# Kernel tuning notes

Hardware: AMD Instinct MI355X
Metric: run time of the kernel (lower is better)

The kernel has to match this reference:

```python
import jax, jax.numpy as jnp
import numpy as np

N_QUBITS = 4
LAYERS = 1

# state has shape [N] + [2]*n; qubit w lives on axis w+1 (wire 0 = most significant, as in PennyLane)

def _apply_ry(state, theta, w, n):
    s0 = jnp.take(state, 0, axis=w + 1)
    s1 = jnp.take(state, 1, axis=w + 1)
    shp = (-1,) + (1,) * (n - 1)
    c = jnp.cos(theta / 2).reshape(shp)
    s = jnp.sin(theta / 2).reshape(shp)
    return jnp.stack([c * s0 - s * s1, s * s0 + c * s1], axis=w + 1)


def _apply_crx(state, theta, ctrl, tgt, n):
    sub0 = jnp.take(state, 0, axis=ctrl + 1)  # control = 0 subspace (unchanged)
    sub1 = jnp.take(state, 1, axis=ctrl + 1)  # control = 1 subspace -> RX on target
    t_ax = tgt + 1 if tgt < ctrl else tgt     # target axis inside sub1 ([N] at axis 0)
    a0 = jnp.take(sub1, 0, axis=t_ax)
    a1 = jnp.take(sub1, 1, axis=t_ax)
    shp = (-1,) + (1,) * (n - 2)
    c = jnp.cos(theta / 2).reshape(shp).astype(state.dtype)
    s = jnp.sin(theta / 2).reshape(shp).astype(state.dtype)
    new1 = jnp.stack([c * a0 - 1j * s * a1, -1j * s * a0 + c * a1], axis=t_ax)
    return jnp.stack([sub0, new1], axis=ctrl + 1)


def run_circuit(params):
    """Ansatz 14 (arXiv:1905.10876) applied to |0...0>, batched over tokens. params: [N, 4*n*layers]."""
    n = N_QUBITS
    N = params.shape[0]
    state = jnp.zeros((N,) + (2,) * n, jnp.complex64)
    state = state.at[(slice(None),) + (0,) * n].set(1.0)
    idx = 0
    for _ in range(LAYERS):
        for i in range(n):
            state = _apply_ry(state, params[:, idx], i, n); idx += 1
        for i in range(n - 1, -1, -1):
            state = _apply_crx(state, params[:, idx], i, (i + 1) % n, n); idx += 1
        for i in range(n):
            state = _apply_ry(state, params[:, idx], i, n); idx += 1
        for i in [n - 1] + list(range(n - 1)):
            state = _apply_crx(state, params[:, idx], i, (i - 1) % n, n); idx += 1
    return state


def measure_xyz(state, n):
    """<X_w>, <Y_w>, <Z_w> for all wires; order matches the PennyLane qnode (all X, all Y, all Z)."""
    N = state.shape[0]
    xs, ys, zs = [], [], []
    for w in range(n):
        s0 = jnp.take(state, 0, axis=w + 1).reshape(N, -1)
        s1 = jnp.take(state, 1, axis=w + 1).reshape(N, -1)
        prod = jnp.sum(jnp.conj(s0) * s1, axis=-1)
        xs.append(2.0 * jnp.real(prod))
        ys.append(2.0 * jnp.imag(prod))
        zs.append(jnp.sum(jnp.abs(s0) ** 2 - jnp.abs(s1) ** 2, axis=-1))
    return jnp.stack(xs + ys + zs, axis=-1)  # [N, 3n]


def setup_inputs() -> dict:
    key = jax.random.key(0)
    k = jax.random.split(key, 7)
    B, L, S, H, E = 2, 2048, 2048, 8, 64
    n_params = 4 * N_QUBITS * LAYERS  # 16
    queries = jax.random.normal(k[0], (B, L, H, E), jnp.float32)
    keys = jax.random.normal(k[1], (B, S, H, E), jnp.float32)
    values = jax.random.normal(k[2], (B, S, H, E), jnp.float32)
    W_angles = jax.random.normal(k[3], (n_params, E), jnp.float32) * 0.125   # Linear(d_model -> 16)
    b_angles = jax.random.normal(k[4], (n_params,), jnp.float32) * 0.125
    W_out = jax.random.normal(k[5], (E, 3 * N_QUBITS), jnp.float32) * 0.28   # Linear(12 -> d_model)
    b_out = jax.random.normal(k[6], (E,), jnp.float32) * 0.28
    return {"queries": queries, "keys": keys, "values": values,
            "W_angles": W_angles, "b_angles": b_angles, "W_out": W_out, "b_out": b_out}


def reference(queries, keys, values, W_angles, b_angles, W_out, b_out):
    B, L, H, E = queries.shape
    S = keys.shape[1]
    scale = 1.0 / np.sqrt(E)
    # quantum encoding of values: angles -> PQC from |0> -> X/Y/Z expvals -> linear map to d_model
    angles = jnp.einsum('bshd,pd->bshp', values, W_angles) + b_angles      # [B,S,H,16]
    state = run_circuit(angles.reshape(-1, angles.shape[-1]))              # [N, 2,2,2,2]
    meas = measure_xyz(state, N_QUBITS)                                    # [N, 12]
    qev = (meas @ W_out.T + b_out).reshape(B, S, H, E)                     # [B,S,H,D]
    # classical attention (eval mode: dropout = identity)
    scores = jnp.einsum('blhe,bshe->bhls', queries, keys)
    mask = jnp.triu(jnp.ones((L, S), bool), 1)
    scores = jnp.where(mask[None, None], -1e9, scores)
    A = jax.nn.softmax(scale * scores, axis=-1)
    return jnp.einsum('bhls,bshd->blhd', A, qev)
```

## Files before the change

### kernel.cpp

```cpp
#include <hip/hip_runtime.h>

#define NP   16
#define EDIM 64
#define HH   8
#define BB   2
#define LL   2048
#define SS   2048
#define NQT  32
#define NPAIR 16
#define LDP  72

typedef __attribute__((ext_vector_type(8))) short bf16x8;
typedef __attribute__((ext_vector_type(4))) float f32x4;

__device__ __forceinline__ float bf2f(unsigned int u) {
    union { unsigned int i; float f; } x; x.i = u << 16; return x.f;
}
__device__ __forceinline__ unsigned short f2bf(float f) {
    union { float ff; unsigned int i; } x; x.ff = f;
    unsigned int r = x.i + 0x7fffu + ((x.i >> 16) & 1u);
    return (unsigned short)(r >> 16);
}
__device__ __forceinline__ unsigned int pk2(float a, float b) {
    return (unsigned int)f2bf(a) | ((unsigned int)f2bf(b) << 16);
}
__device__ __forceinline__ unsigned int tpk2(float a, float b) {
    union { float f; unsigned int i; } xa, xb; xa.f = a; xb.f = b;
    return (xa.i >> 16) | (xb.i & 0xffff0000u);
}

__device__ __forceinline__ void stage16s(const float* __restrict__ g, unsigned short* l, float sc) {
    const float4* gp = (const float4*)g;
    float4 v0 = gp[0], v1 = gp[1], v2 = gp[2], v3 = gp[3];
    uint4 w0, w1;
    w0.x = pk2(v0.x * sc, v0.y * sc); w0.y = pk2(v0.z * sc, v0.w * sc);
    w0.z = pk2(v1.x * sc, v1.y * sc); w0.w = pk2(v1.z * sc, v1.w * sc);
    w1.x = pk2(v2.x * sc, v2.y * sc); w1.y = pk2(v2.z * sc, v2.w * sc);
    w1.z = pk2(v3.x * sc, v3.y * sc); w1.w = pk2(v3.z * sc, v3.w * sc);
    ((uint4*)l)[0] = w0; ((uint4*)l)[1] = w1;
}

#define INV4PI 0.07957747154594767f

__global__ __launch_bounds__(64)
void qev3_kernel(const float* __restrict__ values,
                 const float* __restrict__ key,
                 const float* __restrict__ Wang, const float* __restrict__ bang,
                 const float* __restrict__ Wout, const float* __restrict__ bout,
                 unsigned short* __restrict__ qevb,
                 unsigned short* __restrict__ Kb)
{
    __shared__ float sW[NP * EDIM];
    __shared__ float sWo[EDIM * 12];
    __shared__ float sba[NP];
    __shared__ float sbo[EDIM];

    const int tid = threadIdx.x;
    const int s0  = blockIdx.x * 64;
    const int h   = blockIdx.y;
    const int b   = blockIdx.z;

#pragma unroll
    for (int i = 0; i < 4; i++) ((float4*)sW)[i * 64 + tid] = ((const float4*)Wang)[i * 64 + tid];
#pragma unroll
    for (int i = 0; i < 3; i++) ((float4*)sWo)[i * 64 + tid] = ((const float4*)Wout)[i * 64 + tid];
    if (tid < NP) sba[tid] = bang[tid];
    sbo[tid] = bout[tid];
    __syncthreads();

    const float* vptr = values + ((size_t)(b * SS + s0 + tid) * HH + h) * EDIM;
    float4 vv[16];
#pragma unroll
    for (int c = 0; c < 16; c++) vv[c] = ((const float4*)vptr)[c];

    float ang[NP];
#pragma unroll
    for (int p = 0; p < NP; p++) ang[p] = sba[p];
#pragma unroll
    for (int c = 0; c < 16; c++) {
#pragma unroll
        for (int p = 0; p < NP; p++) {
            float a = ang[p];
            a = fmaf(sW[p * EDIM + c * 4 + 0], vv[c].x, a);
            a = fmaf(sW[p * EDIM + c * 4 + 1], vv[c].y, a);
            a = fmaf(sW[p * EDIM + c * 4 + 2], vv[c].z, a);
            a = fmaf(sW[p * EDIM + c * 4 + 3], vv[c].w, a);
            ang[p] = a;
        }
    }

    float sc[NP], cc[NP];
#pragma unroll
    for (int p = 0; p < NP; p++) {
        float u = ang[p] * INV4PI;
        sc[p] = __builtin_amdgcn_sinf(u);
        cc[p] = __builtin_amdgcn_cosf(u);
    }

    float sr[16], si[16];
#pragma unroll
    for (int i = 0; i < 16; i++) { sr[i] = 0.f; si[i] = 0.f; }
    sr[0] = 1.f;

    auto RY = [&](int w, float s, float c) {
        const int bit = 8 >> w;
#pragma unroll
        for (int i = 0; i < 16; i++) {
            if (!(i & bit)) {
                const int j = i | bit;
                float a0r = sr[i], a0i = si[i], a1r = sr[j], a1i = si[j];
                sr[i] = c * a0r - s * a1r;  si[i] = c * a0i - s * a1i;
                sr[j] = s * a0r + c * a1r;  si[j] = s * a0i + c * a1i;
            }
        }
    };
    auto CRX = [&](int cw, int tw, float s, float c) {
        const int cbit = 8 >> cw, tbit = 8 >> tw;
#pragma unroll
        for (int i = 0; i < 16; i++) {
            if ((i & cbit) && !(i & tbit)) {
                const int j = i | tbit;
                float a0r = sr[i], a0i = si[i], a1r = sr[j], a1i = si[j];
                sr[i] =  c * a0r + s * a1i;  si[i] =  c * a0i - s * a1r;
                sr[j] =  s * a0i + c * a1r;  si[j] = -s * a0r + c * a1i;
            }
        }
    };

    RY(0, sc[0], cc[0]); RY(1, sc[1], cc[1]); RY(2, sc[2], cc[2]); RY(3, sc[3], cc[3]);
    CRX(3, 0, sc[4], cc[4]); CRX(2, 3, sc[5], cc[5]); CRX(1, 2, sc[6], cc[6]); CRX(0, 1, sc[7], cc[7]);
    RY(0, sc[8], cc[8]); RY(1, sc[9], cc[9]); RY(2, sc[10], cc[10]); RY(3, sc[11], cc[11]);
    CRX(3, 2, sc[12], cc[12]); CRX(0, 3, sc[13], cc[13]); CRX(1, 0, sc[14], cc[14]); CRX(2, 1, sc[15], cc[15]);

    float meas[12];
#pragma unroll
    for (int w = 0; w < 4; w++) {
        const int bit = 8 >> w;
        float pr = 0.f, pi = 0.f, z = 0.f;
#pragma unroll
        for (int i = 0; i < 16; i++) {
            if (!(i & bit)) {
                const int j = i | bit;
                pr += sr[i] * sr[j] + si[i] * si[j];
                pi += sr[i] * si[j] - si[i] * sr[j];
                z  += sr[i] * sr[i] + si[i] * si[i] - sr[j] * sr[j] - si[j] * si[j];
            }
        }
        meas[w] = 2.f * pr; meas[4 + w] = 2.f * pi; meas[8 + w] = z;
    }

    unsigned short* ob = qevb + ((size_t)(b * HH + h) * EDIM) * SS + s0 + tid;
#pragma unroll
    for (int eb = 0; eb < 4; eb++) {
        float acc[16];
#pragma unroll
        for (int j = 0; j < 16; j++) acc[j] = sbo[eb * 16 + j];
#pragma unroll
        for (int mm = 0; mm < 12; mm++)
#pragma unroll
            for (int j = 0; j < 16; j++)
                acc[j] = fmaf(meas[mm], sWo[(eb * 16 + j) * 12 + mm], acc[j]);
#pragma unroll
        for (int j = 0; j < 16; j++)
            ob[(size_t)(eb * 16 + j) * SS] = f2bf(acc[j]);
    }

    const float* ks = key + ((size_t)b * SS * HH + h) * EDIM;
    unsigned short* kd = Kb + ((size_t)(b * HH + h) * SS + s0) * EDIM;
#pragma unroll
    for (int i = 0; i < 16; i++) {
        const int u   = i * 64 + tid;
        const int row = u >> 4;
        const int ch  = u & 15;
        float4 v = *(const float4*)(ks + (size_t)(s0 + row) * HH * EDIM + ch * 4);
        uint2 w2; w2.x = pk2(v.x, v.y); w2.y = pk2(v.z, v.w);
        *(uint2*)&kd[row * EDIM + ch * 4] = w2;
    }
}

__global__ __launch_bounds__(256, 1)
void attn6_kernel(const float* __restrict__ qry,
                  const unsigned short* __restrict__ Kb,
                  const unsigned short* __restrict__ Vb,
                  float* __restrict__ out)
{
    __shared__ unsigned short Qs[64 * LDP];
    __shared__ unsigned short Pq[4][64 * LDP];
    __shared__ float Lbuf[16 * 64];

    const int tid  = threadIdx.x;
    const int bx   = blockIdx.x;
    const int h    = blockIdx.y;
    const int b    = blockIdx.z;
    const int w    = tid >> 6;
    const int lane = tid & 63;
    const int ml   = lane & 15;
    const int quad = lane >> 4;
    const int srow = tid >> 2;
    const int sch  = tid & 3;

    const unsigned short* kbase = Kb + (size_t)(b * HH + h) * SS * EDIM;
    const unsigned short* vbase = Vb + (size_t)(b * HH + h) * EDIM * SS;
    unsigned short* Pw = &Pq[w][0];

    for (int pass = 0; pass < 2; ++pass) {
        const int qt = pass ? (NQT - 1 - bx) : bx;
        const int q0 = qt * 64;

        __syncthreads();
        stage16s(qry + (((size_t)b * LL + q0 + srow) * HH + h) * EDIM + sch * 16,
                 &Qs[srow * LDP + sch * 16], 0.125f);
        __syncthreads();

        bf16x8 bq[4][2];
#pragma unroll
        for (int ntq = 0; ntq < 4; ntq++) {
            bq[ntq][0] = *(const bf16x8*)&Qs[(16 * ntq + ml) * LDP + quad * 8];
            bq[ntq][1] = *(const bf16x8*)&Qs[(16 * ntq + ml) * LDP + quad * 8 + 32];
        }

        f32x4 oaccT[4][4];
        float lacc[4] = {0.f, 0.f, 0.f, 0.f};
#pragma unroll
        for (int i = 0; i < 4; i++)
#pragma unroll
            for (int j = 0; j < 4; j++) oaccT[i][j] = (f32x4)(0.f);

        int t = w;
        uint4 kc[8], vc[8];
        if (t <= qt) {
#pragma unroll
            for (int f = 0; f < 8; f++) {
                const int mt = f >> 1, hf = f & 1;
                kc[f] = *(const uint4*)(kbase + (size_t)(t * 64 + 16 * mt + ml) * EDIM + quad * 8 + 32 * hf);
                vc[f] = *(const uint4*)(vbase + (size_t)(16 * mt + ml) * SS + t * 64 + quad * 8 + 32 * hf);
            }
        }

        for (; t <= qt; t += 4) {
            uint4 kn[8], vn[8];
            const bool more = (t + 4 <= qt);
            if (more) {
#pragma unroll
                for (int f = 0; f < 8; f++) {
                    const int mt = f >> 1, hf = f & 1;
                    kn[f] = *(const uint4*)(kbase + (size_t)((t + 4) * 64 + 16 * mt + ml) * EDIM + quad * 8 + 32 * hf);
                    vn[f] = *(const uint4*)(vbase + (size_t)(16 * mt + ml) * SS + (t + 4) * 64 + quad * 8 + 32 * hf);
                }
            }
            const bool diag = (t == qt);

#pragma unroll
            for (int mts = 0; mts < 4; mts++)
#pragma unroll
                for (int ntq = 0; ntq < 4; ntq++) {
                    f32x4 s = __builtin_amdgcn_mfma_f32_16x16x32_bf16(
                        *(const bf16x8*)&kc[2 * mts], bq[ntq][0], (f32x4)(0.f), 0, 0, 0);
                    s = __builtin_amdgcn_mfma_f32_16x16x32_bf16(
                        *(const bf16x8*)&kc[2 * mts + 1], bq[ntq][1], s, 0, 0, 0);
                    float p0 = __expf(s[0]), p1 = __expf(s[1]), p2 = __expf(s[2]), p3 = __expf(s[3]);
                    if (diag) {
                        const int sbase = 16 * mts + 4 * quad, qcol = 16 * ntq + ml;
                        if (sbase + 0 > qcol) p0 = 0.f;
                        if (sbase + 1 > qcol) p1 = 0.f;
                        if (sbase + 2 > qcol) p2 = 0.f;
                        if (sbase + 3 > qcol) p3 = 0.f;
                    }
                    lacc[ntq] += (p0 + p1) + (p2 + p3);
                    uint2 u; u.x = tpk2(p0, p1); u.y = tpk2(p2, p3);
                    *(uint2*)&Pw[(16 * ntq + ml) * LDP + 16 * mts + 4 * quad] = u;
                }

#pragma unroll
            for (int ntq = 0; ntq < 4; ntq++) {
                bf16x8 pb0 = *(const bf16x8*)&Pw[(16 * ntq + ml) * LDP + quad * 8];
                bf16x8 pb1 = *(const bf16x8*)&Pw[(16 * ntq + ml) * LDP + quad * 8 + 32];
#pragma unroll
                for (int mte = 0; mte < 4; mte++) {
                    oaccT[mte][ntq] = __builtin_amdgcn_mfma_f32_16x16x32_bf16(
                        *(const bf16x8*)&vc[2 * mte], pb0, oaccT[mte][ntq], 0, 0, 0);
                    oaccT[mte][ntq] = __builtin_amdgcn_mfma_f32_16x16x32_bf16(
                        *(const bf16x8*)&vc[2 * mte + 1], pb1, oaccT[mte][ntq], 0, 0, 0);
                }
            }

            if (more) {
#pragma unroll
                for (int f = 0; f < 8; f++) { kc[f] = kn[f]; vc[f] = vn[f]; }
            }
        }

#pragma unroll
        for (int mte = 0; mte < 4; mte++)
#pragma unroll
            for (int ntq = 0; ntq < 4; ntq++) {
                uint2 u;
                u.x = pk2(oaccT[mte][ntq][0], oaccT[mte][ntq][1]);
                u.y = pk2(oaccT[mte][ntq][2], oaccT[mte][ntq][3]);
                *(uint2*)&Pw[(16 * ntq + ml) * LDP + 16 * mte + 4 * quad] = u;
            }
#pragma unroll
        for (int ntq = 0; ntq < 4; ntq++)
            Lbuf[(w * 4 + quad) * 64 + 16 * ntq + ml] = lacc[ntq];

        __syncthreads();

        {
            const int q = tid >> 2, c = tid & 3;
            float lsum = 0.f;
#pragma unroll
            for (int i = 0; i < 16; i++) lsum += Lbuf[i * 64 + q];
            const float inv = 1.f / lsum;
            float* orow = out + (((size_t)b * LL + q0 + q) * HH + h) * EDIM;
#pragma unroll
            for (int c4 = 0; c4 < 4; c4++) {
                const int e0 = c * 16 + c4 * 4;
                float a0 = 0.f, a1 = 0.f, a2 = 0.f, a3 = 0.f;
#pragma unroll
                for (int wv = 0; wv < 4; wv++) {
                    uint2 u = *(const uint2*)&Pq[wv][q * LDP + e0];
                    a0 += bf2f(u.x & 0xffffu); a1 += bf2f(u.x >> 16);
                    a2 += bf2f(u.y & 0xffffu); a3 += bf2f(u.y >> 16);
                }
                float4 r; r.x = a0 * inv; r.y = a1 * inv; r.z = a2 * inv; r.w = a3 * inv;
                *(float4*)&orow[e0] = r;
            }
        }
    }
}

extern "C" void kernel_launch(void* const* d_in, const int* in_sizes, int n_in,
                              void* d_out, int out_size, void* d_ws, size_t ws_size,
                              hipStream_t stream)
{
    const float* qry  = (const float*)d_in[0];
    const float* key  = (const float*)d_in[1];
    const float* val  = (const float*)d_in[2];
    const float* Wang = (const float*)d_in[3];
    const float* bang = (const float*)d_in[4];
    const float* Wout = (const float*)d_in[5];
    const float* bout = (const float*)d_in[6];
    float* out = (float*)d_out;

    unsigned short* qevb = (unsigned short*)d_ws;
    unsigned short* Kb   = (unsigned short*)((char*)d_ws + (size_t)BB * HH * EDIM * SS * 2);

    (void)in_sizes; (void)n_in; (void)out_size; (void)ws_size;

    qev3_kernel<<<dim3(SS / 64, HH, BB), 64, 0, stream>>>(val, key, Wang, bang, Wout, bout, qevb, Kb);
    attn6_kernel<<<dim3(NPAIR, HH, BB), 256, 0, stream>>>(qry, Kb, qevb, out);
}
```

Before: 119.1 us.

## Split qev work four threads per token and double attention waves to eight

```diff
diff --git a/kernel.cpp b/kernel.cpp
--- a/kernel.cpp
+++ b/kernel.cpp
@@ -9,6 +9,7 @@
 #define NQT  32
 #define NPAIR 16
 #define LDP  72
+#define NW   8
 
 typedef __attribute__((ext_vector_type(8))) short bf16x8;
 typedef __attribute__((ext_vector_type(4))) float f32x4;
@@ -42,51 +43,42 @@
 
 #define INV4PI 0.07957747154594767f
 
-__global__ __launch_bounds__(64)
-void qev3_kernel(const float* __restrict__ values,
+__global__ __launch_bounds__(256)
+void qev4_kernel(const float* __restrict__ values,
                  const float* __restrict__ key,
                  const float* __restrict__ Wang, const float* __restrict__ bang,
                  const float* __restrict__ Wout, const float* __restrict__ bout,
                  unsigned short* __restrict__ qevb,
                  unsigned short* __restrict__ Kb)
 {
-    __shared__ float sW[NP * EDIM];
-    __shared__ float sWo[EDIM * 12];
-    __shared__ float sba[NP];
-    __shared__ float sbo[EDIM];
-
-    const int tid = threadIdx.x;
-    const int s0  = blockIdx.x * 64;
-    const int h   = blockIdx.y;
-    const int b   = blockIdx.z;
-
-#pragma unroll
-    for (int i = 0; i < 4; i++) ((float4*)sW)[i * 64 + tid] = ((const float4*)Wang)[i * 64 + tid];
-#pragma unroll
-    for (int i = 0; i < 3; i++) ((float4*)sWo)[i * 64 + tid] = ((const float4*)Wout)[i * 64 + tid];
-    if (tid < NP) sba[tid] = bang[tid];
-    sbo[tid] = bout[tid];
-    __syncthreads();
-
-    const float* vptr = values + ((size_t)(b * SS + s0 + tid) * HH + h) * EDIM;
-    float4 vv[16];
-#pragma unroll
-    for (int c = 0; c < 16; c++) vv[c] = ((const float4*)vptr)[c];
+    const int tid   = threadIdx.x;
+    const int s0    = blockIdx.x * 64;
+    const int h     = blockIdx.y;
+    const int b     = blockIdx.z;
+    const int token = s0 + (tid >> 2);
+    const int p4    = tid & 3;
+
+    const float* vptr = values + ((size_t)(b * SS + token) * HH + h) * EDIM + p4 * 16;
+    float4 vv[4];
+#pragma unroll
+    for (int c = 0; c < 4; c++) vv[c] = ((const float4*)vptr)[c];
 
     float ang[NP];
 #pragma unroll
-    for (int p = 0; p < NP; p++) ang[p] = sba[p];
-#pragma unroll
-    for (int c = 0; c < 16; c++) {
-#pragma unroll
-        for (int p = 0; p < NP; p++) {
-            float a = ang[p];
-            a = fmaf(sW[p * EDIM + c * 4 + 0], vv[c].x, a);
-            a = fmaf(sW[p * EDIM + c * 4 + 1], vv[c].y, a);
-            a = fmaf(sW[p * EDIM + c * 4 + 2], vv[c].z, a);
-            a = fmaf(sW[p * EDIM + c * 4 + 3], vv[c].w, a);
-            ang[p] = a;
-        }
+    for (int p = 0; p < NP; p++) {
+        const float4* wp = (const float4*)(Wang + p * EDIM + p4 * 16);
+        float a = 0.f;
+#pragma unroll
+        for (int c = 0; c < 4; c++) {
+            float4 w = wp[c];
+            a = fmaf(w.x, vv[c].x, a);
+            a = fmaf(w.y, vv[c].y, a);
+            a = fmaf(w.z, vv[c].z, a);
+            a = fmaf(w.w, vv[c].w, a);
+        }
+        a += __shfl_xor(a, 1, 64);
+        a += __shfl_xor(a, 2, 64);
+        ang[p] = a + bang[p];
     }
 
     float sc[NP], cc[NP];
@@ -149,27 +141,29 @@
         meas[w] = 2.f * pr; meas[4 + w] = 2.f * pi; meas[8 + w] = z;
     }
 
-    unsigned short* ob = qevb + ((size_t)(b * HH + h) * EDIM) * SS + s0 + tid;
-#pragma unroll
-    for (int eb = 0; eb < 4; eb++) {
-        float acc[16];
-#pragma unroll
-        for (int j = 0; j < 16; j++) acc[j] = sbo[eb * 16 + j];
-#pragma unroll
-        for (int mm = 0; mm < 12; mm++)
-#pragma unroll
-            for (int j = 0; j < 16; j++)
-                acc[j] = fmaf(meas[mm], sWo[(eb * 16 + j) * 12 + mm], acc[j]);
-#pragma unroll
-        for (int j = 0; j < 16; j++)
-            ob[(size_t)(eb * 16 + j) * SS] = f2bf(acc[j]);
+    unsigned short* ob = qevb + ((size_t)(b * HH + h) * EDIM) * SS + token;
+    const float4* bo4 = (const float4*)(bout + p4 * 16);
+    float4 bo[4] = { bo4[0], bo4[1], bo4[2], bo4[3] };
+#pragma unroll
+    for (int j = 0; j < 16; j++) {
+        const int e = p4 * 16 + j;
+        const float4* wr = (const float4*)(Wout + e * 12);
+        float4 w0 = wr[0], w1 = wr[1], w2 = wr[2];
+        float a = ((const float*)bo)[j];
+        a = fmaf(meas[0], w0.x, a);  a = fmaf(meas[1],  w0.y, a);
+        a = fmaf(meas[2], w0.z, a);  a = fmaf(meas[3],  w0.w, a);
+        a = fmaf(meas[4], w1.x, a);  a = fmaf(meas[5],  w1.y, a);
+        a = fmaf(meas[6], w1.z, a);  a = fmaf(meas[7],  w1.w, a);
+        a = fmaf(meas[8], w2.x, a);  a = fmaf(meas[9],  w2.y, a);
+        a = fmaf(meas[10], w2.z, a); a = fmaf(meas[11], w2.w, a);
+        ob[(size_t)e * SS] = f2bf(a);
     }
 
     const float* ks = key + ((size_t)b * SS * HH + h) * EDIM;
     unsigned short* kd = Kb + ((size_t)(b * HH + h) * SS + s0) * EDIM;
 #pragma unroll
-    for (int i = 0; i < 16; i++) {
-        const int u   = i * 64 + tid;
+    for (int i = 0; i < 4; i++) {
+        const int u   = i * 256 + tid;
         const int row = u >> 4;
         const int ch  = u & 15;
         float4 v = *(const float4*)(ks + (size_t)(s0 + row) * HH * EDIM + ch * 4);
@@ -178,15 +172,16 @@
     }
 }
 
-__global__ __launch_bounds__(256, 1)
-void attn6_kernel(const float* __restrict__ qry,
+__global__ __launch_bounds__(512, 1)
+void attn7_kernel(const float* __restrict__ qry,
                   const unsigned short* __restrict__ Kb,
                   const unsigned short* __restrict__ Vb,
                   float* __restrict__ out)
 {
-    __shared__ unsigned short Qs[64 * LDP];
-    __shared__ unsigned short Pq[4][64 * LDP];
-    __shared__ float Lbuf[16 * 64];
+    extern __shared__ unsigned short smem[];
+    unsigned short* Qs = smem;
+    unsigned short* Pq = smem + 64 * LDP;
+    float* Lbuf = (float*)(smem + (1 + NW) * 64 * LDP);
 
     const int tid  = threadIdx.x;
     const int bx   = blockIdx.x;
@@ -196,20 +191,21 @@
     const int lane = tid & 63;
     const int ml   = lane & 15;
     const int quad = lane >> 4;
-    const int srow = tid >> 2;
-    const int sch  = tid & 3;
 
     const unsigned short* kbase = Kb + (size_t)(b * HH + h) * SS * EDIM;
     const unsigned short* vbase = Vb + (size_t)(b * HH + h) * EDIM * SS;
-    unsigned short* Pw = &Pq[w][0];
+    unsigned short* Pw = Pq + w * 64 * LDP;
 
     for (int pass = 0; pass < 2; ++pass) {
         const int qt = pass ? (NQT - 1 - bx) : bx;
         const int q0 = qt * 64;
 
         __syncthreads();
-        stage16s(qry + (((size_t)b * LL + q0 + srow) * HH + h) * EDIM + sch * 16,
-                 &Qs[srow * LDP + sch * 16], 0.125f);
+        if (tid < 256) {
+            const int srow = tid >> 2, sch = tid & 3;
+            stage16s(qry + (((size_t)b * LL + q0 + srow) * HH + h) * EDIM + sch * 16,
+                     &Qs[srow * LDP + sch * 16], 0.125f);
+        }
         __syncthreads();
 
         bf16x8 bq[4][2];
@@ -237,15 +233,15 @@
             }
         }
 
-        for (; t <= qt; t += 4) {
+        for (; t <= qt; t += NW) {
             uint4 kn[8], vn[8];
-            const bool more = (t + 4 <= qt);
+            const bool more = (t + NW <= qt);
             if (more) {
 #pragma unroll
                 for (int f = 0; f < 8; f++) {
                     const int mt = f >> 1, hf = f & 1;
-                    kn[f] = *(const uint4*)(kbase + (size_t)((t + 4) * 64 + 16 * mt + ml) * EDIM + quad * 8 + 32 * hf);
-                    vn[f] = *(const uint4*)(vbase + (size_t)(16 * mt + ml) * SS + (t + 4) * 64 + quad * 8 + 32 * hf);
+                    kn[f] = *(const uint4*)(kbase + (size_t)((t + NW) * 64 + 16 * mt + ml) * EDIM + quad * 8 + 32 * hf);
+                    vn[f] = *(const uint4*)(vbase + (size_t)(16 * mt + ml) * SS + (t + NW) * 64 + quad * 8 + 32 * hf);
                 }
             }
             const bool diag = (t == qt);
@@ -306,19 +302,19 @@
         __syncthreads();
 
         {
-            const int q = tid >> 2, c = tid & 3;
+            const int q = tid >> 3, c = tid & 7;
             float lsum = 0.f;
 #pragma unroll
-            for (int i = 0; i < 16; i++) lsum += Lbuf[i * 64 + q];
+            for (int i = 0; i < 4 * NW; i++) lsum += Lbuf[i * 64 + q];
             const float inv = 1.f / lsum;
             float* orow = out + (((size_t)b * LL + q0 + q) * HH + h) * EDIM;
 #pragma unroll
-            for (int c4 = 0; c4 < 4; c4++) {
-                const int e0 = c * 16 + c4 * 4;
+            for (int c4 = 0; c4 < 2; c4++) {
+                const int e0 = c * 8 + c4 * 4;
                 float a0 = 0.f, a1 = 0.f, a2 = 0.f, a3 = 0.f;
 #pragma unroll
-                for (int wv = 0; wv < 4; wv++) {
-                    uint2 u = *(const uint2*)&Pq[wv][q * LDP + e0];
+                for (int wv = 0; wv < NW; wv++) {
+                    uint2 u = *(const uint2*)&Pq[wv * 64 * LDP + q * LDP + e0];
                     a0 += bf2f(u.x & 0xffffu); a1 += bf2f(u.x >> 16);
                     a2 += bf2f(u.y & 0xffffu); a3 += bf2f(u.y >> 16);
                 }
@@ -347,6 +343,8 @@
 
     (void)in_sizes; (void)n_in; (void)out_size; (void)ws_size;
 
-    qev3_kernel<<<dim3(SS / 64, HH, BB), 64, 0, stream>>>(val, key, Wang, bang, Wout, bout, qevb, Kb);
-    attn6_kernel<<<dim3(NPAIR, HH, BB), 256, 0, stream>>>(qry, Kb, qevb, out);
-}
+    const size_t smem = (size_t)(1 + NW) * 64 * LDP * 2 + (size_t)4 * NW * 64 * 4;
+
+    qev4_kernel<<<dim3(SS / 64, HH, BB), 256, 0, stream>>>(val, key, Wang, bang, Wout, bout, qevb, Kb);
+    attn7_kernel<<<dim3(NPAIR, HH, BB), 512, smem, stream>>>(qry, Kb, qevb, out);
+}
```

Measured after the change: 164.0 us. 37.7% more time.
